# Optimization experiments

Measured on AMD Instinct MI355X. Metric: run time of the kernel, lower is better.

## Reference

```python
import jax, jax.numpy as jnp
import numpy as np

B, S, HID = 1, 2048, 2048
H, NOPE, ROPE, VDIM = 16, 128, 64, 128
QR, KVR = 1536, 512
IH, ID = 16, 128
TOPK = 512
THETA = 10000.0
EPS = 1e-6
SCALE = (NOPE + ROPE) ** -0.5
NEG = -1e9


def _cos_sin(s, dim, dtype):
    inv = 1.0 / (THETA ** (np.arange(0, dim, 2, dtype=np.float32) / dim))
    t = np.arange(s, dtype=np.float32)
    f = np.outer(t, inv)
    emb = np.concatenate([f, f], -1)
    return jnp.asarray(np.cos(emb), dtype), jnp.asarray(np.sin(emb), dtype)


def _rope(x, cos, sin):
    # x: [b,s,h,d]; cos/sin: [s,d]; NeoX-style rotate_half
    x1, x2 = jnp.split(x, 2, axis=-1)
    rot = jnp.concatenate([-x2, x1], axis=-1)
    return x * cos[None, :, None, :] + rot * sin[None, :, None, :]


def _rmsnorm(x, w):
    v = jnp.mean(x.astype(jnp.float32) ** 2, -1, keepdims=True)
    return (x.astype(jnp.float32) * jax.lax.rsqrt(v + EPS)).astype(x.dtype) * w


def _layernorm(x, w, b):
    m = jnp.mean(x, -1, keepdims=True)
    v = jnp.var(x, -1, keepdims=True)
    return (x - m) * jax.lax.rsqrt(v + EPS) * w + b


def setup_inputs() -> dict:
    key = jax.random.key(0)
    ks = jax.random.split(key, 12)
    g = lambda k, shp: jax.random.normal(k, shp, jnp.float32) * 0.02
    return {
        'hidden_states': jax.random.normal(ks[0], (B, S, HID), jnp.float32),
        'q_a_w': g(ks[1], (QR, HID)),
        'q_a_ln_w': jnp.ones((QR,), jnp.float32),
        'q_b_w': g(ks[2], (H * (NOPE + ROPE), QR)),
        'kv_a_w': g(ks[3], (KVR + ROPE, HID)),
        'kv_a_ln_w': jnp.ones((KVR,), jnp.float32),
        'kv_b_w': g(ks[4], (H * (NOPE + VDIM), KVR)),
        'o_w': g(ks[5], (HID, H * VDIM)),
        'idx_wq_b_w': g(ks[6], (IH * ID, QR)),
        'idx_wk_w': g(ks[7], (ID, HID)),
        'idx_kn_w': jnp.ones((ID,), jnp.float32),
        'idx_kn_b': jnp.zeros((ID,), jnp.float32),
        'idx_wproj_w': g(ks[8], (IH, HID)),
    }


def reference(hidden_states, q_a_w, q_a_ln_w, q_b_w, kv_a_w, kv_a_ln_w, kv_b_w, o_w,
              idx_wq_b_w, idx_wk_w, idx_kn_w, idx_kn_b, idx_wproj_w):
    b, s, _ = hidden_states.shape
    cos, sin = _cos_sin(s, ROPE, hidden_states.dtype)

    # --- MLA projections ---
    qr = _rmsnorm(hidden_states @ q_a_w.T, q_a_ln_w)                 # [b,s,QR]
    q = (qr @ q_b_w.T).reshape(b, s, H, NOPE + ROPE)
    q_nope, q_pe = q[..., :NOPE], q[..., NOPE:]
    q_pe = _rope(q_pe, cos, sin)
    ckv = hidden_states @ kv_a_w.T                                   # [b,s,KVR+ROPE]
    c_kv, k_pe = ckv[..., :KVR], ckv[..., KVR:]
    k_pe = _rope(k_pe[:, :, None, :], cos, sin)                      # [b,s,1,ROPE]
    kv = (_rmsnorm(c_kv, kv_a_ln_w) @ kv_b_w.T).reshape(b, s, H, NOPE + VDIM)
    k_nope, v = kv[..., :NOPE], kv[..., NOPE:]

    # --- DSA indexer: per-token importance scores ---
    iq = (qr @ idx_wq_b_w.T).reshape(b, s, IH, ID)
    iq = jnp.concatenate([_rope(iq[..., :ROPE], cos, sin), iq[..., ROPE:]], -1)
    ik = _layernorm(hidden_states @ idx_wk_w.T, idx_kn_w, idx_kn_b)  # [b,s,ID]
    ik_pe = _rope(ik[:, :, None, :ROPE], cos, sin)[:, :, 0, :]
    ik = jnp.concatenate([ik_pe, ik[..., ROPE:]], -1)
    iw = (hidden_states @ idx_wproj_w.T) * (IH ** -0.5)              # [b,s,IH]
    idx_scores = jnp.einsum('bqh,bhqk->bqk', iw,
                            jax.nn.relu(jnp.einsum('bqhd,bkd->bhqk', iq, ik)))
    causal = jnp.tril(jnp.ones((s, s), bool))
    idx_scores = jnp.where(causal[None], idx_scores, -jnp.inf)
    _, top_idx = jax.lax.top_k(idx_scores, TOPK)                     # [b,s,TOPK]
    bi = jnp.arange(b)[:, None, None]
    qi = jnp.arange(s)[None, :, None]
    keep = jnp.zeros((b, s, s), bool).at[bi, qi, top_idx].set(True)
    allowed = keep & causal[None]                                    # [b,s,s]

    # --- sparse top-k attention (top-k mask to -inf before softmax) ---
    qh = jnp.concatenate([q_nope, q_pe], -1)                         # [b,s,H,192]
    kh = jnp.concatenate([k_nope, jnp.broadcast_to(k_pe, (b, s, H, ROPE))], -1)
    scores = jnp.einsum('bqhd,bkhd->bhqk', qh, kh) * SCALE
    scores = jnp.where(allowed[:, None], scores, NEG)
    attn = jax.nn.softmax(scores, -1)
    out = jnp.einsum('bhqk,bkhd->bqhd', attn, v).reshape(b, s, H * VDIM)
    return out @ o_w.T
```

## Files before the change

### kernel.cpp

```cpp
#include <hip/hip_runtime.h>
#include <hip/hip_bf16.h>
#include <math.h>

#define SEQ 2048
#define HIDD 2048
#define QRANK 1536
#define KVRANK 512
#define TOPK 512
#define EPSF 1e-6f
#define SCALE_ATTN 0.07216878364870323f
#define NCAT 1680

typedef __attribute__((ext_vector_type(8))) short short8v;
typedef __attribute__((ext_vector_type(4))) short short4v;
typedef __attribute__((ext_vector_type(4))) float f32x4;

__device__ inline unsigned short f2bf(float f) {
    unsigned u = __float_as_uint(f);
    unsigned r = (u + 0x7FFFu + ((u >> 16) & 1u)) >> 16;
    return (unsigned short)r;
}
__device__ inline float bf2f(unsigned short b) {
    return __uint_as_float(((unsigned)b) << 16);
}
__device__ inline void split2(float x, unsigned short& h, unsigned short& l) {
    h = f2bf(x);
    l = f2bf(x - bf2f(h));
}

__device__ inline short4v ds_read_tr16(const void* p) {
#if __has_builtin(__builtin_amdgcn_ds_read_tr16_b64)
    return __builtin_amdgcn_ds_read_tr16_b64((short4v*)p);
#else
    const unsigned short* u = (const unsigned short*)p;
    short4v r;
    r[0] = (short)u[0]; r[1] = (short)u[16]; r[2] = (short)u[32]; r[3] = (short)u[48];
    return r;
#endif
}

__global__ void rope_table_kernel(float* __restrict__ cos_t, float* __restrict__ sin_t) {
    int s = blockIdx.x;
    int i = threadIdx.x;
    double inv = pow(10000.0, -((double)(2 * i)) / 64.0);
    double f = (double)s * inv;
    cos_t[s * 32 + i] = (float)cos(f);
    sin_t[s * 32 + i] = (float)sin(f);
}

__global__ __launch_bounds__(256) void cvt_bf16_kernel(const float* __restrict__ in,
                                                       unsigned short* __restrict__ out, int n4) {
    for (int i = blockIdx.x * 256 + threadIdx.x; i < n4; i += gridDim.x * 256) {
        float4 v = ((const float4*)in)[i];
        ushort4 o;
        o.x = f2bf(v.x); o.y = f2bf(v.y); o.z = f2bf(v.z); o.w = f2bf(v.w);
        ((ushort4*)out)[i] = o;
    }
}

__global__ __launch_bounds__(256) void wkt_kernel(const float* __restrict__ kvb,
                                                  unsigned short* __restrict__ wkt) {
    int o = blockIdx.x * 256 + threadIdx.x;
    int d = o & 127;
    int n = (o >> 7) & 511;
    int h = o >> 16;
    wkt[o] = f2bf(kvb[((size_t)(h * 256 + d)) * 512 + n]);
}

__global__ __launch_bounds__(256) void khg_kernel(const float* __restrict__ ckvn,
                                                  const float* __restrict__ ckv,
                                                  unsigned short* __restrict__ khg) {
    int s = blockIdx.x;
    for (int i = threadIdx.x; i < 576; i += 256) {
        float v = (i < 512) ? ckvn[(size_t)s * 512 + i] : ckv[(size_t)s * 576 + i];
        khg[(size_t)s * 576 + i] = f2bf(v);
    }
}

__global__ __launch_bounds__(256) void gemm_cat_split_kernel(
    const float* __restrict__ hidden, const float* __restrict__ q_a_w,
    const float* __restrict__ idx_wk_w, const float* __restrict__ idx_wproj_w,
    float* __restrict__ ccat)
{
    __shared__ __align__(16) unsigned short Ah[128 * 32], Al[128 * 32];
    __shared__ __align__(16) unsigned short Bh[128 * 32], Bl[128 * 32];
    int tid = threadIdx.x;
    int l = tid & 63, w = tid >> 6;
    int wr = w >> 1, wc = w & 1;
    int m0 = blockIdx.x * 128, n0 = blockIdx.y * 128;
    f32x4 acc[4][4] = {};
    for (int k0 = 0; k0 < HIDD; k0 += 32) {
        __syncthreads();
#pragma unroll
        for (int i = 0; i < 2; ++i) {
            int idx = tid + i * 256;
            int r = idx >> 2, cc = idx & 3;
            int sw = cc ^ (r & 3);
            {
                const float* src = hidden + (size_t)(m0 + r) * HIDD + k0 + cc * 8;
                float4 f0 = *(const float4*)src, f1 = *(const float4*)(src + 4);
                float xs[8] = {f0.x, f0.y, f0.z, f0.w, f1.x, f1.y, f1.z, f1.w};
                short8v dh, dl;
#pragma unroll
                for (int e = 0; e < 8; ++e) {
                    unsigned short hh, ll; split2(xs[e], hh, ll);
                    dh[e] = (short)hh; dl[e] = (short)ll;
                }
                *(short8v*)&Ah[r * 32 + sw * 8] = dh;
                *(short8v*)&Al[r * 32 + sw * 8] = dl;
            }
            {
                int gb = n0 + r; if (gb > NCAT - 1) gb = NCAT - 1;
                float scale = 1.f;
                const float* src;
                if (gb < 1536) src = q_a_w + (size_t)gb * HIDD;
                else if (gb < 1664) src = idx_wk_w + (size_t)(gb - 1536) * HIDD;
                else { src = idx_wproj_w + (size_t)(gb - 1664) * HIDD; scale = 0.25f; }
                src += k0 + cc * 8;
                float4 f0 = *(const float4*)src, f1 = *(const float4*)(src + 4);
                float xs[8] = {f0.x, f0.y, f0.z, f0.w, f1.x, f1.y, f1.z, f1.w};
                short8v dh, dl;
#pragma unroll
                for (int e = 0; e < 8; ++e) {
                    unsigned short hh, ll; split2(xs[e] * scale, hh, ll);
                    dh[e] = (short)hh; dl[e] = (short)ll;
                }
                *(short8v*)&Bh[r * 32 + sw * 8] = dh;
                *(short8v*)&Bl[r * 32 + sw * 8] = dl;
            }
        }
        __syncthreads();
        short8v avh[4], avl[4];
#pragma unroll
        for (int mt = 0; mt < 4; ++mt) {
            int row = wr * 64 + mt * 16 + (l & 15);
            int ch = (l >> 4) ^ (row & 3);
            avh[mt] = *(const short8v*)&Ah[row * 32 + ch * 8];
            avl[mt] = *(const short8v*)&Al[row * 32 + ch * 8];
        }
#pragma unroll
        for (int nt = 0; nt < 4; ++nt) {
            int row = wc * 64 + nt * 16 + (l & 15);
            int ch = (l >> 4) ^ (row & 3);
            short8v bvh = *(const short8v*)&Bh[row * 32 + ch * 8];
            short8v bvl = *(const short8v*)&Bl[row * 32 + ch * 8];
#pragma unroll
            for (int mt = 0; mt < 4; ++mt) {
                acc[mt][nt] = __builtin_amdgcn_mfma_f32_16x16x32_bf16(avh[mt], bvh, acc[mt][nt], 0, 0, 0);
                acc[mt][nt] = __builtin_amdgcn_mfma_f32_16x16x32_bf16(avh[mt], bvl, acc[mt][nt], 0, 0, 0);
                acc[mt][nt] = __builtin_amdgcn_mfma_f32_16x16x32_bf16(avl[mt], bvh, acc[mt][nt], 0, 0, 0);
            }
        }
    }
#pragma unroll
    for (int mt = 0; mt < 4; ++mt)
#pragma unroll
        for (int nt = 0; nt < 4; ++nt)
#pragma unroll
            for (int i = 0; i < 4; ++i) {
                int gm = m0 + wr * 64 + mt * 16 + (l >> 4) * 4 + i;
                int gn = n0 + wc * 64 + nt * 16 + (l & 15);
                if (gn < NCAT) ccat[(size_t)gm * NCAT + gn] = acc[mt][nt][i];
            }
}

__global__ __launch_bounds__(256) void gemm_iq_split_kernel(
    const float* __restrict__ qr, const float* __restrict__ wq,
    const float* __restrict__ cos_t, const float* __restrict__ sin_t,
    unsigned short* __restrict__ iqh, unsigned short* __restrict__ iql)
{
    __shared__ __align__(16) unsigned short Ah[128 * 32], Al[128 * 32];
    __shared__ __align__(16) unsigned short Bh[128 * 32], Bl[128 * 32];
    int tid = threadIdx.x;
    int l = tid & 63, w = tid >> 6;
    int wr = w >> 1, wc = w & 1;
    int m0 = blockIdx.x * 128, n0 = blockIdx.y * 128;
    int hh_ = blockIdx.y;
    f32x4 acc[4][4] = {};
    for (int k0 = 0; k0 < QRANK; k0 += 32) {
        __syncthreads();
#pragma unroll
        for (int i = 0; i < 2; ++i) {
            int idx = tid + i * 256;
            int r = idx >> 2, cc = idx & 3;
            int sw = cc ^ (r & 3);
            {
                const float* src = qr + (size_t)(m0 + r) * QRANK + k0 + cc * 8;
                float4 f0 = *(const float4*)src, f1 = *(const float4*)(src + 4);
                float xs[8] = {f0.x, f0.y, f0.z, f0.w, f1.x, f1.y, f1.z, f1.w};
                short8v dh, dl;
#pragma unroll
                for (int e = 0; e < 8; ++e) {
                    unsigned short h2, l2; split2(xs[e], h2, l2);
                    dh[e] = (short)h2; dl[e] = (short)l2;
                }
                *(short8v*)&Ah[r * 32 + sw * 8] = dh;
                *(short8v*)&Al[r * 32 + sw * 8] = dl;
            }
            {
                const float* src = wq + (size_t)(n0 + r) * QRANK + k0 + cc * 8;
                float4 f0 = *(const float4*)src, f1 = *(const float4*)(src + 4);
                float xs[8] = {f0.x, f0.y, f0.z, f0.w, f1.x, f1.y, f1.z, f1.w};
                short8v dh, dl;
#pragma unroll
                for (int e = 0; e < 8; ++e) {
                    unsigned short h2, l2; split2(xs[e], h2, l2);
                    dh[e] = (short)h2; dl[e] = (short)l2;
                }
                *(short8v*)&Bh[r * 32 + sw * 8] = dh;
                *(short8v*)&Bl[r * 32 + sw * 8] = dl;
            }
        }
        __syncthreads();
        short8v avh[4], avl[4];
#pragma unroll
        for (int mt = 0; mt < 4; ++mt) {
            int row = wr * 64 + mt * 16 + (l & 15);
            int ch = (l >> 4) ^ (row & 3);
            avh[mt] = *(const short8v*)&Ah[row * 32 + ch * 8];
            avl[mt] = *(const short8v*)&Al[row * 32 + ch * 8];
        }
#pragma unroll
        for (int nt = 0; nt < 4; ++nt) {
            int row = wc * 64 + nt * 16 + (l & 15);
            int ch = (l >> 4) ^ (row & 3);
            short8v bvh = *(const short8v*)&Bh[row * 32 + ch * 8];
            short8v bvl = *(const short8v*)&Bl[row * 32 + ch * 8];
#pragma unroll
            for (int mt = 0; mt < 4; ++mt) {
                acc[mt][nt] = __builtin_amdgcn_mfma_f32_16x16x32_bf16(avh[mt], bvh, acc[mt][nt], 0, 0, 0);
                acc[mt][nt] = __builtin_amdgcn_mfma_f32_16x16x32_bf16(avh[mt], bvl, acc[mt][nt], 0, 0, 0);
                acc[mt][nt] = __builtin_amdgcn_mfma_f32_16x16x32_bf16(avl[mt], bvh, acc[mt][nt], 0, 0, 0);
            }
        }
    }
    if (wc == 0) {
#pragma unroll
        for (int mt = 0; mt < 4; ++mt)
#pragma unroll
            for (int nt = 0; nt < 2; ++nt)
#pragma unroll
                for (int i = 0; i < 4; ++i) {
                    int q = m0 + wr * 64 + mt * 16 + (l >> 4) * 4 + i;
                    int dd = nt * 16 + (l & 15);
                    float c = cos_t[q * 32 + dd], s = sin_t[q * 32 + dd];
                    float x1 = acc[mt][nt][i], x2 = acc[mt][nt + 2][i];
                    acc[mt][nt][i] = x1 * c - x2 * s;
                    acc[mt][nt + 2][i] = x2 * c + x1 * s;
                }
    }
#pragma unroll
    for (int mt = 0; mt < 4; ++mt)
#pragma unroll
        for (int nt = 0; nt < 4; ++nt)
#pragma unroll
            for (int i = 0; i < 4; ++i) {
                int q = m0 + wr * 64 + mt * 16 + (l >> 4) * 4 + i;
                int d = wc * 64 + nt * 16 + (l & 15);
                size_t idx = ((size_t)q * 16 + hh_) * 128 + d;
                unsigned short h2, l2; split2(acc[mt][nt][i], h2, l2);
                iqh[idx] = h2; iql[idx] = l2;
            }
}

template <typename TA, typename TC>
__global__ __launch_bounds__(256) void mfma_nt_kernel(
    const TA* __restrict__ A, const unsigned short* __restrict__ B, TC* __restrict__ C,
    int M, int N, int K, int lda, int ldb, int ldc, long ab, long bb, long cb)
{
    __shared__ __align__(16) unsigned short Asl[128 * 32];
    __shared__ __align__(16) unsigned short Bsl[128 * 32];
    int z = blockIdx.z;
    const TA* Az = A + (size_t)z * ab;
    const unsigned short* Bz = B + (size_t)z * bb;
    TC* Cz = C + (size_t)z * cb;
    int tid = threadIdx.x;
    int l = tid & 63, w = tid >> 6;
    int wr = w >> 1, wc = w & 1;
    int m0 = blockIdx.x * 128, n0 = blockIdx.y * 128;
    f32x4 acc[4][4] = {};

    for (int k0 = 0; k0 < K; k0 += 32) {
        __syncthreads();
#pragma unroll
        for (int i = 0; i < 2; ++i) {
            int idx = tid + i * 256;
            int r = idx >> 2, cc = idx & 3;
            int sw = cc ^ (r & 3);
            {
                short8v d;
                const TA* src = Az + (size_t)(m0 + r) * lda + k0 + cc * 8;
                if constexpr (sizeof(TA) == 2) {
                    d = *(const short8v*)src;
                } else {
                    float4 f0 = *(const float4*)src;
                    float4 f1 = *(const float4*)(src + 4);
                    d[0] = (short)f2bf(f0.x); d[1] = (short)f2bf(f0.y);
                    d[2] = (short)f2bf(f0.z); d[3] = (short)f2bf(f0.w);
                    d[4] = (short)f2bf(f1.x); d[5] = (short)f2bf(f1.y);
                    d[6] = (short)f2bf(f1.z); d[7] = (short)f2bf(f1.w);
                }
                *(short8v*)&Asl[r * 32 + sw * 8] = d;
            }
            {
                int gb = n0 + r; if (gb > N - 1) gb = N - 1;
                short8v d = *(const short8v*)(Bz + (size_t)gb * ldb + k0 + cc * 8);
                *(short8v*)&Bsl[r * 32 + sw * 8] = d;
            }
        }
        __syncthreads();
        short8v av[4], bv[4];
#pragma unroll
        for (int mt = 0; mt < 4; ++mt) {
            int row = wr * 64 + mt * 16 + (l & 15);
            int ch = (l >> 4) ^ (row & 3);
            av[mt] = *(const short8v*)&Asl[row * 32 + ch * 8];
        }
#pragma unroll
        for (int nt = 0; nt < 4; ++nt) {
            int row = wc * 64 + nt * 16 + (l & 15);
            int ch = (l >> 4) ^ (row & 3);
            bv[nt] = *(const short8v*)&Bsl[row * 32 + ch * 8];
        }
#pragma unroll
        for (int mt = 0; mt < 4; ++mt)
#pragma unroll
            for (int nt = 0; nt < 4; ++nt)
                acc[mt][nt] = __builtin_amdgcn_mfma_f32_16x16x32_bf16(av[mt], bv[nt], acc[mt][nt], 0, 0, 0);
    }
#pragma unroll
    for (int mt = 0; mt < 4; ++mt) {
#pragma unroll
        for (int nt = 0; nt < 4; ++nt) {
#pragma unroll
            for (int i = 0; i < 4; ++i) {
                int gm = m0 + wr * 64 + mt * 16 + (l >> 4) * 4 + i;
                int gn = n0 + wc * 64 + nt * 16 + (l & 15);
                if (gn < N) {
                    float v = acc[mt][nt][i];
                    if constexpr (sizeof(TC) == 4) Cz[(size_t)gm * ldc + gn] = v;
                    else Cz[(size_t)gm * ldc + gn] = f2bf(v);
                }
            }
        }
    }
}

__global__ __launch_bounds__(256) void rmsnorm_kernel(
    const float* __restrict__ in, const float* __restrict__ w, float* __restrict__ out,
    unsigned short* __restrict__ bf_out, int n, int in_stride)
{
    int row = blockIdx.x, tid = threadIdx.x;
    const float* x = in + (size_t)row * in_stride;
    float4 v[2];
    int cnt = 0;
    float ss = 0.f;
    int nf4 = n >> 2;
    for (int i = tid; i < nf4; i += 256) {
        float4 t = *(const float4*)(x + i * 4);
        v[cnt++] = t;
        ss += t.x * t.x + t.y * t.y + t.z * t.z + t.w * t.w;
    }
#pragma unroll
    for (int m = 32; m; m >>= 1) ss += __shfl_xor(ss, m);
    __shared__ float red[8];
    int wid = tid >> 6;
    if ((tid & 63) == 0) red[wid] = ss;
    __syncthreads();
    if (tid == 0) {
        float s = red[0] + red[1] + red[2] + red[3];
        red[4] = rsqrtf(s / (float)n + EPSF);
    }
    __syncthreads();
    float scale = red[4];
    cnt = 0;
    for (int i = tid; i < nf4; i += 256) {
        float4 t = v[cnt++];
        float4 wv = *(const float4*)(w + i * 4);
        float4 o;
        o.x = t.x * scale * wv.x; o.y = t.y * scale * wv.y;
        o.z = t.z * scale * wv.z; o.w = t.w * scale * wv.w;
        *(float4*)(out + (size_t)row * n + i * 4) = o;
        if (bf_out) {
            ushort4 ob;
            ob.x = f2bf(o.x); ob.y = f2bf(o.y); ob.z = f2bf(o.z); ob.w = f2bf(o.w);
            *(ushort4*)(bf_out + (size_t)row * n + i * 4) = ob;
        }
    }
}

__global__ __launch_bounds__(64) void ln_rope_split_kernel(
    const float* __restrict__ in, int stride,
    const float* __restrict__ w, const float* __restrict__ b,
    const float* __restrict__ cos_t, const float* __restrict__ sin_t,
    unsigned short* __restrict__ ikh, unsigned short* __restrict__ ikl)
{
    int row = blockIdx.x, tid = threadIdx.x;
    const float* x = in + (size_t)row * stride;
    float x0 = x[tid], x1 = x[tid + 64];
    float s = x0 + x1, ss = x0 * x0 + x1 * x1;
#pragma unroll
    for (int m = 32; m; m >>= 1) { s += __shfl_xor(s, m); ss += __shfl_xor(ss, m); }
    float mean = s * (1.f / 128.f);
    float var = ss * (1.f / 128.f) - mean * mean;
    float r = rsqrtf(var + EPSF);
    float n0 = (x0 - mean) * r * w[tid] + b[tid];
    float n1 = (x1 - mean) * r * w[tid + 64] + b[tid + 64];
    float c = cos_t[row * 32 + (tid & 31)], sn = sin_t[row * 32 + (tid & 31)];
    float other = __shfl_xor(n0, 32);
    float r0 = (tid < 32) ? (n0 * c - other * sn) : (n0 * c + other * sn);
    unsigned short h2, l2;
    split2(r0, h2, l2);
    ikh[(size_t)row * 128 + tid] = h2; ikl[(size_t)row * 128 + tid] = l2;
    split2(n1, h2, l2);
    ikh[(size_t)row * 128 + 64 + tid] = h2; ikl[(size_t)row * 128 + 64 + tid] = l2;
}

__global__ void rope_apply_kernel(
    float* __restrict__ x, const float* __restrict__ cos_t, const float* __restrict__ sin_t,
    int heads, int row_stride, int head_stride, int offset)
{
    int t = blockIdx.x * blockDim.x + threadIdx.x;
    int i = t & 31;
    int hh = (t >> 5) % heads;
    int r = t / (32 * heads);
    if (r >= SEQ) return;
    float* p = x + (size_t)r * row_stride + hh * head_stride + offset;
    float c = cos_t[r * 32 + i], s = sin_t[r * 32 + i];
    float x1 = p[i], x2 = p[i + 32];
    p[i] = x1 * c - x2 * s;
    p[i + 32] = x2 * c + x1 * s;
}

__global__ __launch_bounds__(256) void idx_scores_mfma_kernel(
    const unsigned short* __restrict__ iqh, const unsigned short* __restrict__ iql,
    const unsigned short* __restrict__ ikh, const unsigned short* __restrict__ ikl,
    const float* __restrict__ iwsrc, int iw_stride,
    float* __restrict__ scores)
{
    int q0 = blockIdx.x * 64, k0 = blockIdx.y * 64;
    int tid = threadIdx.x;
    if (k0 > q0 + 63) {
        for (int t = tid; t < 64 * 64; t += 256) {
            int r = t >> 6, c = t & 63;
            scores[(size_t)(q0 + r) * SEQ + k0 + c] = -INFINITY;
        }
        return;
    }
    __shared__ __align__(16) unsigned short skh[64 * 128], skl[64 * 128];
    __shared__ __align__(16) unsigned short sqh[64 * 128], sql[64 * 128];
    __shared__ float iws[64][16];
    int l = tid & 63, w = tid >> 6;
    for (int it = tid; it < 64 * 16; it += 256) {
        int r = it >> 4, c = it & 15;
        int sw = c ^ (r & 15);
        *(short8v*)&skh[r * 128 + sw * 8] = *(const short8v*)(ikh + (size_t)(k0 + r) * 128 + c * 8);
        *(short8v*)&skl[r * 128 + sw * 8] = *(const short8v*)(ikl + (size_t)(k0 + r) * 128 + c * 8);
    }
    {
        int r = tid >> 2, c = tid & 3;
        *(float4*)&iws[r][c * 4] = *(const float4*)(iwsrc + (size_t)(q0 + r) * iw_stride + c * 4);
    }
    f32x4 acc[4] = {};
    for (int h = 0; h < 16; ++h) {
        __syncthreads();
        for (int it = tid; it < 64 * 16; it += 256) {
            int r = it >> 4, c = it & 15;
            int sw = c ^ (r & 15);
            size_t base = ((size_t)(q0 + r) * 16 + h) * 128 + c * 8;
            *(short8v*)&sqh[r * 128 + sw * 8] = *(const short8v*)(iqh + base);
            *(short8v*)&sql[r * 128 + sw * 8] = *(const short8v*)(iql + base);
        }
        __syncthreads();
        f32x4 dot[4] = {};
#pragma unroll
        for (int ks = 0; ks < 4; ++ks) {
            int arow = w * 16 + (l & 15);
            int ach = ((l >> 4) + ks * 4) ^ (arow & 15);
            short8v ah = *(const short8v*)&sqh[arow * 128 + ach * 8];
            short8v al = *(const short8v*)&sql[arow * 128 + ach * 8];
#pragma unroll
            for (int nt = 0; nt < 4; ++nt) {
                int brow = nt * 16 + (l & 15);
                int bch = ((l >> 4) + ks * 4) ^ (brow & 15);
                short8v bh = *(const short8v*)&skh[brow * 128 + bch * 8];
                short8v bl = *(const short8v*)&skl[brow * 128 + bch * 8];
                dot[nt] = __builtin_amdgcn_mfma_f32_16x16x32_bf16(ah, bh, dot[nt], 0, 0, 0);
                dot[nt] = __builtin_amdgcn_mfma_f32_16x16x32_bf16(ah, bl, dot[nt], 0, 0, 0);
                dot[nt] = __builtin_amdgcn_mfma_f32_16x16x32_bf16(al, bh, dot[nt], 0, 0, 0);
            }
        }
#pragma unroll
        for (int nt = 0; nt < 4; ++nt)
#pragma unroll
            for (int i = 0; i < 4; ++i) {
                float wv = iws[w * 16 + (l >> 4) * 4 + i][h];
                acc[nt][i] += wv * fmaxf(dot[nt][i], 0.f);
            }
    }
#pragma unroll
    for (int nt = 0; nt < 4; ++nt)
#pragma unroll
        for (int i = 0; i < 4; ++i) {
            int q = q0 + w * 16 + (l >> 4) * 4 + i;
            int k = k0 + nt * 16 + (l & 15);
            scores[(size_t)q * SEQ + k] = (k <= q) ? acc[nt][i] : -INFINITY;
        }
}

__global__ __launch_bounds__(1024) void topk_kernel(
    const float* __restrict__ scores, int* __restrict__ sel)
{
    int qi = blockIdx.x, tid = threadIdx.x;
    __shared__ unsigned long long keys[2048];
    const float* srow = scores + (size_t)qi * SEQ;
#pragma unroll
    for (int r = 0; r < 2; ++r) {
        int k = tid + r * 1024;
        unsigned u = __float_as_uint(srow[k]);
        unsigned mv = (u & 0x80000000u) ? ~u : (u | 0x80000000u);
        keys[k] = ((unsigned long long)mv << 32) | (unsigned)(2047 - k);
    }
    for (int ksz = 2; ksz <= 2048; ksz <<= 1) {
        for (int j = ksz >> 1; j > 0; j >>= 1) {
            __syncthreads();
#pragma unroll 1
            for (int r = 0; r < 2; ++r) {
                int i = tid + r * 1024;
                int ixj = i ^ j;
                if (ixj > i) {
                    unsigned long long a = keys[i], b = keys[ixj];
                    bool dir = ((i & ksz) == 0);
                    if ((a < b) == dir) { keys[i] = b; keys[ixj] = a; }
                }
            }
        }
    }
    __syncthreads();
    if (tid < TOPK) {
        int k = 2047 - (int)(keys[tid] & 0xFFFFFFFFu);
        sel[(size_t)qi * TOPK + tid] = (tid <= qi) ? k : -1;
    }
}

__global__ __launch_bounds__(256) void attn_mfma_kernel(
    const unsigned short* __restrict__ qabs,
    const float* __restrict__ qsrc,
    const unsigned short* __restrict__ khg,
    const int* __restrict__ sel,
    unsigned short* __restrict__ ocomp)
{
    __shared__ __align__(16) char smem[77568];
    unsigned short* plds = (unsigned short*)(smem + 74752);
    float* smax = (float*)(smem + 76800);
    float* ssum = (float*)(smem + 77056);
    int* selb   = (int*)(smem + 77312);

    const int qi = blockIdx.x;
    const int tid = threadIdx.x;
    const int l = tid & 63, w = tid >> 6;
    const int lg = l >> 4, lr = l & 15;
    const int nv = min(TOPK, qi + 1);
    const int ntile = (nv + 63) >> 6;
    const int krow = w * 16 + lr;

    short8v aq[18];
    {
        const unsigned short* qa = qabs + ((size_t)qi * 16 + lr) * 512 + lg * 8;
#pragma unroll
        for (int ks = 0; ks < 16; ++ks)
            aq[ks] = *(const short8v*)(qa + ks * 32);
        const float* qp = qsrc + (size_t)qi * 3072 + lr * 192 + 128 + lg * 8;
#pragma unroll
        for (int ks = 0; ks < 2; ++ks) {
            float4 f0 = *(const float4*)(qp + ks * 32);
            float4 f1 = *(const float4*)(qp + ks * 32 + 4);
            short8v d;
            d[0] = (short)f2bf(f0.x); d[1] = (short)f2bf(f0.y);
            d[2] = (short)f2bf(f0.z); d[3] = (short)f2bf(f0.w);
            d[4] = (short)f2bf(f1.x); d[5] = (short)f2bf(f1.y);
            d[6] = (short)f2bf(f1.z); d[7] = (short)f2bf(f1.w);
            aq[16 + ks] = d;
        }
    }

    const int sbase = krow * 32 + (lg >> 1) * 2080 + (lg & 1) * 16;
    const int vboff = w * 16640 + lg * 256 + lr * 2;

    float m[4] = {-1e30f, -1e30f, -1e30f, -1e30f};
    float lsum[4] = {0.f, 0.f, 0.f, 0.f};
    f32x4 oacc[8] = {};

    for (int t = 0; t < ntile; ++t) {
        const int j0 = t * 64;
        __syncthreads();
        if (tid < 64) {
            int sv = sel[(size_t)qi * TOPK + j0 + tid];
            selb[tid] = sv < 0 ? 0 : sv;
        }
        __syncthreads();
        for (int it = tid; it < 64 * 64; it += 256) {
            int key = it >> 6, c = it & 63;
            short8v v = *(const short8v*)(khg + (size_t)selb[key] * 576 + c * 8);
            *(short8v*)(smem + (c >> 1) * 2080 + key * 32 + (c & 1) * 16) = v;
        }
        for (int it = tid; it < 64 * 8; it += 256) {
            int key = it >> 3, c = it & 7;
            short8v v = *(const short8v*)(khg + (size_t)selb[key] * 576 + 512 + c * 8);
            *(short8v*)(smem + 66560 + ((key * 128 + c * 16) ^ ((key & 7) << 4))) = v;
        }
        __syncthreads();
        f32x4 s = {};
#pragma unroll
        for (int ks = 0; ks < 16; ++ks) {
            short8v b = *(const short8v*)(smem + sbase + ks * 4160);
            s = __builtin_amdgcn_mfma_f32_16x16x32_bf16(aq[ks], b, s, 0, 0, 0);
        }
#pragma unroll
        for (int ks = 0; ks < 2; ++ks) {
            short8v b = *(const short8v*)(smem + 66560 +
                ((krow * 128 + ks * 64 + lg * 16) ^ ((krow & 7) << 4)));
            s = __builtin_amdgcn_mfma_f32_16x16x32_bf16(aq[16 + ks], b, s, 0, 0, 0);
        }
        bool kvalid = (j0 + krow) < nv;
#pragma unroll
        for (int i = 0; i < 4; ++i)
            s[i] = kvalid ? s[i] * SCALE_ATTN : -1e30f;
        float tm[4];
#pragma unroll
        for (int i = 0; i < 4; ++i) tm[i] = s[i];
#pragma unroll
        for (int sh = 1; sh < 16; sh <<= 1)
#pragma unroll
            for (int i = 0; i < 4; ++i) tm[i] = fmaxf(tm[i], __shfl_xor(tm[i], sh));
        if (lr == 0) *(float4*)&smax[w * 16 + lg * 4] = make_float4(tm[0], tm[1], tm[2], tm[3]);
        __syncthreads();
        float mn[4], scl[4];
#pragma unroll
        for (int i = 0; i < 4; ++i) {
            int h = lg * 4 + i;
            float tmax = fmaxf(fmaxf(smax[h], smax[16 + h]), fmaxf(smax[32 + h], smax[48 + h]));
            mn[i] = fmaxf(m[i], tmax);
            scl[i] = __expf(m[i] - mn[i]);
            m[i] = mn[i];
        }
        float p[4], rs[4];
#pragma unroll
        for (int i = 0; i < 4; ++i) { p[i] = __expf(s[i] - mn[i]); rs[i] = p[i]; }
#pragma unroll
        for (int sh = 1; sh < 16; sh <<= 1)
#pragma unroll
            for (int i = 0; i < 4; ++i) rs[i] += __shfl_xor(rs[i], sh);
        if (lr == 0) *(float4*)&ssum[w * 16 + lg * 4] = make_float4(rs[0], rs[1], rs[2], rs[3]);
        {
            ushort4 pb;
            pb.x = f2bf(p[0]); pb.y = f2bf(p[1]); pb.z = f2bf(p[2]); pb.w = f2bf(p[3]);
            *(ushort4*)&plds[(w * 16 + lr) * 16 + lg * 4] = pb;
        }
        __syncthreads();
#pragma unroll
        for (int i = 0; i < 4; ++i) {
            int h = lg * 4 + i;
            float ts = ssum[h] + ssum[16 + h] + ssum[32 + h] + ssum[48 + h];
            lsum[i] = lsum[i] * scl[i] + ts;
        }
#pragma unroll
        for (int nt = 0; nt < 8; ++nt)
#pragma unroll
            for (int i = 0; i < 4; ++i) oacc[nt][i] *= scl[i];
#pragma unroll
        for (int kb = 0; kb < 2; ++kb) {
            short8v af;
#pragma unroll
            for (int j = 0; j < 8; ++j)
                af[j] = (short)plds[(kb * 32 + lg * 8 + j) * 16 + lr];
#pragma unroll
            for (int nt = 0; nt < 8; ++nt) {
                const char* a = smem + vboff + kb * 1024 + nt * 2080;
                short4v t0 = ds_read_tr16(a);
                short4v t1 = ds_read_tr16(a + 128);
                short8v bf = __builtin_shufflevector(t0, t1, 0, 1, 2, 3, 4, 5, 6, 7);
                oacc[nt] = __builtin_amdgcn_mfma_f32_16x16x32_bf16(af, bf, oacc[nt], 0, 0, 0);
            }
        }
    }
    float inv[4];
#pragma unroll
    for (int i = 0; i < 4; ++i) inv[i] = 1.f / lsum[i];
    unsigned short* ob = ocomp + (size_t)qi * 16 * 512;
#pragma unroll
    for (int nt = 0; nt < 8; ++nt) {
        int d = w * 128 + nt * 16 + lr;
#pragma unroll
        for (int i = 0; i < 4; ++i) {
            int h = lg * 4 + i;
            ob[h * 512 + d] = f2bf(oacc[nt][i] * inv[i]);
        }
    }
}

extern "C" void kernel_launch(void* const* d_in, const int* in_sizes, int n_in,
                              void* d_out, int out_size, void* d_ws, size_t ws_size,
                              hipStream_t stream) {
    (void)in_sizes; (void)n_in; (void)out_size; (void)ws_size;
    const float* hidden      = (const float*)d_in[0];
    const float* q_a_w       = (const float*)d_in[1];
    const float* q_a_ln_w    = (const float*)d_in[2];
    const float* q_b_w       = (const float*)d_in[3];
    const float* kv_a_w      = (const float*)d_in[4];
    const float* kv_a_ln_w   = (const float*)d_in[5];
    const float* kv_b_w      = (const float*)d_in[6];
    const float* o_w         = (const float*)d_in[7];
    const float* idx_wq_b_w  = (const float*)d_in[8];
    const float* idx_wk_w    = (const float*)d_in[9];
    const float* idx_kn_w    = (const float*)d_in[10];
    const float* idx_kn_b    = (const float*)d_in[11];
    const float* idx_wproj_w = (const float*)d_in[12];
    float* out = (float*)d_out;

    char* ws = (char*)d_ws;
    size_t off = 0;
    auto alloc = [&](size_t nbytes) -> void* {
        void* p = ws + off;
        off = (off + nbytes + 255) & ~(size_t)255;
        return p;
    };
    float* cos_t = (float*)alloc((size_t)SEQ * 32 * 4);
    float* sin_t = (float*)alloc((size_t)SEQ * 32 * 4);
    float* qbuf  = (float*)alloc((size_t)SEQ * 3072 * 4);
    float* ckv   = (float*)alloc((size_t)SEQ * 576 * 4);
    float* ckvn  = (float*)alloc((size_t)SEQ * KVRANK * 4);
    int*   sel   = (int*)alloc((size_t)SEQ * TOPK * 4);
    unsigned short* khg      = (unsigned short*)alloc((size_t)SEQ * 576 * 2);
    unsigned short* attno_bf = (unsigned short*)alloc((size_t)SEQ * 2048 * 2);
    unsigned short* qr_bf    = (unsigned short*)alloc((size_t)SEQ * QRANK * 2);
    unsigned short* q_b_bf   = (unsigned short*)alloc((size_t)3072 * QRANK * 2);
    unsigned short* kv_a_bf  = (unsigned short*)alloc((size_t)576 * HIDD * 2);
    unsigned short* o_w_bf   = (unsigned short*)alloc((size_t)HIDD * 2048 * 2);
    unsigned short* kv_b_bf  = (unsigned short*)alloc((size_t)4096 * 512 * 2);
    unsigned short* wkt      = (unsigned short*)alloc((size_t)16 * 512 * 128 * 2);
    size_t mark = off;
    float* qr    = (float*)alloc((size_t)SEQ * QRANK * 4);
    float* ccat  = (float*)alloc((size_t)SEQ * NCAT * 4);
    float* scores = (float*)alloc((size_t)SEQ * SEQ * 4);
    unsigned short* iqh = (unsigned short*)alloc((size_t)SEQ * 2048 * 2);
    unsigned short* iql = (unsigned short*)alloc((size_t)SEQ * 2048 * 2);
    unsigned short* ikh = (unsigned short*)alloc((size_t)SEQ * 128 * 2);
    unsigned short* ikl = (unsigned short*)alloc((size_t)SEQ * 128 * 2);
    off = mark;
    unsigned short* qabsb = (unsigned short*)alloc((size_t)SEQ * 16 * 512 * 2);
    unsigned short* ocomp = (unsigned short*)alloc((size_t)SEQ * 16 * 512 * 2);

    rope_table_kernel<<<dim3(SEQ), dim3(32), 0, stream>>>(cos_t, sin_t);

    cvt_bf16_kernel<<<1024, 256, 0, stream>>>(q_b_w, q_b_bf, 3072 * QRANK / 4);
    cvt_bf16_kernel<<<1024, 256, 0, stream>>>(kv_a_w, kv_a_bf, 576 * HIDD / 4);
    cvt_bf16_kernel<<<1024, 256, 0, stream>>>(o_w, o_w_bf, HIDD * 2048 / 4);
    cvt_bf16_kernel<<<1024, 256, 0, stream>>>(kv_b_w, kv_b_bf, 4096 * 512 / 4);
    wkt_kernel<<<4096, 256, 0, stream>>>(kv_b_w, wkt);

    gemm_cat_split_kernel<<<dim3(16, 14), 256, 0, stream>>>(hidden, q_a_w, idx_wk_w, idx_wproj_w, ccat);

    rmsnorm_kernel<<<SEQ, 256, 0, stream>>>(ccat, q_a_ln_w, qr, qr_bf, QRANK, NCAT);

    ln_rope_split_kernel<<<SEQ, 64, 0, stream>>>(ccat + 1536, NCAT, idx_kn_w, idx_kn_b, cos_t, sin_t, ikh, ikl);

    mfma_nt_kernel<unsigned short, float><<<dim3(16, 24, 1), 256, 0, stream>>>(
        qr_bf, q_b_bf, qbuf, SEQ, 3072, QRANK, QRANK, QRANK, 3072, 0L, 0L, 0L);
    rope_apply_kernel<<<(SEQ * 16 * 32) / 256, 256, 0, stream>>>(qbuf, cos_t, sin_t, 16, 3072, 192, 128);

    mfma_nt_kernel<float, float><<<dim3(16, 5, 1), 256, 0, stream>>>(
        hidden, kv_a_bf, ckv, SEQ, 576, HIDD, HIDD, HIDD, 576, 0L, 0L, 0L);
    rope_apply_kernel<<<(SEQ * 32) / 256, 256, 0, stream>>>(ckv, cos_t, sin_t, 1, 576, 0, 512);
    rmsnorm_kernel<<<SEQ, 256, 0, stream>>>(ckv, kv_a_ln_w, ckvn, nullptr, KVRANK, 576);
    khg_kernel<<<SEQ, 256, 0, stream>>>(ckvn, ckv, khg);

    gemm_iq_split_kernel<<<dim3(16, 16), 256, 0, stream>>>(qr, idx_wq_b_w, cos_t, sin_t, iqh, iql);

    idx_scores_mfma_kernel<<<dim3(32, 32), 256, 0, stream>>>(iqh, iql, ikh, ikl, ccat + 1664, NCAT, scores);
    topk_kernel<<<SEQ, 1024, 0, stream>>>(scores, sel);

    mfma_nt_kernel<float, unsigned short><<<dim3(16, 4, 16), 256, 0, stream>>>(
        qbuf, wkt, qabsb, SEQ, 512, 128, 3072, 128, 16 * 512,
        192L, 512L * 128L, 512L);

    attn_mfma_kernel<<<SEQ, 256, 0, stream>>>(qabsb, qbuf, khg, sel, ocomp);

    mfma_nt_kernel<unsigned short, unsigned short><<<dim3(16, 1, 16), 256, 0, stream>>>(
        ocomp, kv_b_bf + (size_t)128 * 512, attno_bf, SEQ, 128, 512,
        16 * 512, 512, 2048, 512L, 256L * 512L, 128L);

    mfma_nt_kernel<unsigned short, float><<<dim3(16, 16, 1), 256, 0, stream>>>(
        attno_bf, o_w_bf, out, SEQ, HIDD, 2048, 2048, 2048, HIDD, 0L, 0L, 0L);
}
```

Before: 926.7 us.

## Fuse RoPE into GEMM epilogues, merge rmsnorm+bf16 pack, retile attention to 32-key tiles

Applies rotary embedding inside the mfma GEMM epilogue for the q_b and kv_a projections, which removes the separate rope_apply passes over qbuf and ckv. RMSNorm and the bf16 packing of the latent KV are merged into one kernel, dropping the ckvn intermediate. The wkt transpose now goes through a shared-memory tile to get coalesced accesses. The sparse attention kernel moves from 64-key to 32-key tiles with half the LDS, with two waves computing scores under raised priority. This trades more tile iterations and some idle waves for higher occupancy.

```diff
diff --git a/kernel.cpp b/kernel.cpp
--- a/kernel.cpp
+++ b/kernel.cpp
@@ -60,20 +60,22 @@
 
 __global__ __launch_bounds__(256) void wkt_kernel(const float* __restrict__ kvb,
                                                   unsigned short* __restrict__ wkt) {
-    int o = blockIdx.x * 256 + threadIdx.x;
-    int d = o & 127;
-    int n = (o >> 7) & 511;
-    int h = o >> 16;
-    wkt[o] = f2bf(kvb[((size_t)(h * 256 + d)) * 512 + n]);
-}
-
-__global__ __launch_bounds__(256) void khg_kernel(const float* __restrict__ ckvn,
-                                                  const float* __restrict__ ckv,
-                                                  unsigned short* __restrict__ khg) {
-    int s = blockIdx.x;
-    for (int i = threadIdx.x; i < 576; i += 256) {
-        float v = (i < 512) ? ckvn[(size_t)s * 512 + i] : ckv[(size_t)s * 576 + i];
-        khg[(size_t)s * 576 + i] = f2bf(v);
+    __shared__ float t[128][129];
+    int h = blockIdx.x, n0 = blockIdx.y * 128;
+    int tid = threadIdx.x;
+    for (int it = tid; it < 128 * 32; it += 256) {
+        int d = it >> 5, c4 = it & 31;
+        float4 v = *(const float4*)(kvb + ((size_t)(h * 256 + d)) * 512 + n0 + c4 * 4);
+        t[d][c4 * 4 + 0] = v.x; t[d][c4 * 4 + 1] = v.y;
+        t[d][c4 * 4 + 2] = v.z; t[d][c4 * 4 + 3] = v.w;
+    }
+    __syncthreads();
+    for (int it = tid; it < 128 * 32; it += 256) {
+        int n = it >> 5, dc = it & 31;
+        ushort4 o;
+        o.x = f2bf(t[dc * 4 + 0][n]); o.y = f2bf(t[dc * 4 + 1][n]);
+        o.z = f2bf(t[dc * 4 + 2][n]); o.w = f2bf(t[dc * 4 + 3][n]);
+        *(ushort4*)(wkt + ((size_t)h * 512 + n0 + n) * 128 + dc * 4) = o;
     }
 }
 
@@ -266,7 +268,8 @@
 template <typename TA, typename TC>
 __global__ __launch_bounds__(256) void mfma_nt_kernel(
     const TA* __restrict__ A, const unsigned short* __restrict__ B, TC* __restrict__ C,
-    int M, int N, int K, int lda, int ldb, int ldc, long ab, long bb, long cb)
+    int M, int N, int K, int lda, int ldb, int ldc, long ab, long bb, long cb,
+    const float* __restrict__ cos_t, const float* __restrict__ sin_t, int rope_mode)
 {
     __shared__ __align__(16) unsigned short Asl[128 * 32];
     __shared__ __align__(16) unsigned short Bsl[128 * 32];
@@ -328,6 +331,25 @@
             for (int nt = 0; nt < 4; ++nt)
                 acc[mt][nt] = __builtin_amdgcn_mfma_f32_16x16x32_bf16(av[mt], bv[nt], acc[mt][nt], 0, 0, 0);
     }
+    if (rope_mode) {
+        int gcol64 = (n0 >> 6) + wc;
+        bool dorope = (rope_mode == 1) ? ((gcol64 % 3) == 2) : (gcol64 == 8);
+        if (dorope) {
+#pragma unroll
+            for (int mt = 0; mt < 4; ++mt)
+#pragma unroll
+                for (int nt = 0; nt < 2; ++nt)
+#pragma unroll
+                    for (int i = 0; i < 4; ++i) {
+                        int q = m0 + wr * 64 + mt * 16 + (l >> 4) * 4 + i;
+                        int dd = nt * 16 + (l & 15);
+                        float c = cos_t[q * 32 + dd], sn = sin_t[q * 32 + dd];
+                        float x1 = acc[mt][nt][i], x2 = acc[mt][nt + 2][i];
+                        acc[mt][nt][i] = x1 * c - x2 * sn;
+                        acc[mt][nt + 2][i] = x2 * c + x1 * sn;
+                    }
+        }
+    }
 #pragma unroll
     for (int mt = 0; mt < 4; ++mt) {
 #pragma unroll
@@ -389,6 +411,37 @@
     }
 }
 
+__global__ __launch_bounds__(256) void rmsnorm_khg_kernel(
+    const float* __restrict__ ckv, const float* __restrict__ w,
+    unsigned short* __restrict__ khg)
+{
+    int row = blockIdx.x, tid = threadIdx.x;
+    const float* x = ckv + (size_t)row * 576;
+    float4 v = make_float4(0.f, 0.f, 0.f, 0.f);
+    float ss = 0.f;
+    if (tid < 128) {
+        v = *(const float4*)(x + tid * 4);
+        ss = v.x * v.x + v.y * v.y + v.z * v.z + v.w * v.w;
+    }
+#pragma unroll
+    for (int mm = 32; mm; mm >>= 1) ss += __shfl_xor(ss, mm);
+    __shared__ float red[8];
+    if ((tid & 63) == 0) red[tid >> 6] = ss;
+    __syncthreads();
+    if (tid == 0) red[4] = rsqrtf((red[0] + red[1] + red[2] + red[3]) * (1.f / 512.f) + EPSF);
+    __syncthreads();
+    float scale = red[4];
+    if (tid < 128) {
+        float4 wv = *(const float4*)(w + tid * 4);
+        ushort4 ob;
+        ob.x = f2bf(v.x * scale * wv.x); ob.y = f2bf(v.y * scale * wv.y);
+        ob.z = f2bf(v.z * scale * wv.z); ob.w = f2bf(v.w * scale * wv.w);
+        *(ushort4*)(khg + (size_t)row * 576 + tid * 4) = ob;
+    } else if (tid < 192) {
+        khg[(size_t)row * 576 + 512 + (tid - 128)] = f2bf(x[512 + tid - 128]);
+    }
+}
+
 __global__ __launch_bounds__(64) void ln_rope_split_kernel(
     const float* __restrict__ in, int stride,
     const float* __restrict__ w, const float* __restrict__ b,
@@ -416,22 +469,6 @@
     ikh[(size_t)row * 128 + 64 + tid] = h2; ikl[(size_t)row * 128 + 64 + tid] = l2;
 }
 
-__global__ void rope_apply_kernel(
-    float* __restrict__ x, const float* __restrict__ cos_t, const float* __restrict__ sin_t,
-    int heads, int row_stride, int head_stride, int offset)
-{
-    int t = blockIdx.x * blockDim.x + threadIdx.x;
-    int i = t & 31;
-    int hh = (t >> 5) % heads;
-    int r = t / (32 * heads);
-    if (r >= SEQ) return;
-    float* p = x + (size_t)r * row_stride + hh * head_stride + offset;
-    float c = cos_t[r * 32 + i], s = sin_t[r * 32 + i];
-    float x1 = p[i], x2 = p[i + 32];
-    p[i] = x1 * c - x2 * s;
-    p[i + 32] = x2 * c + x1 * s;
-}
-
 __global__ __launch_bounds__(256) void idx_scores_mfma_kernel(
     const unsigned short* __restrict__ iqh, const unsigned short* __restrict__ iql,
     const unsigned short* __restrict__ ikh, const unsigned short* __restrict__ ikl,
@@ -550,18 +587,18 @@
     const int* __restrict__ sel,
     unsigned short* __restrict__ ocomp)
 {
-    __shared__ __align__(16) char smem[77568];
-    unsigned short* plds = (unsigned short*)(smem + 74752);
-    float* smax = (float*)(smem + 76800);
-    float* ssum = (float*)(smem + 77056);
-    int* selb   = (int*)(smem + 77312);
+    __shared__ __align__(16) char smem[39424];
+    unsigned short* plds = (unsigned short*)(smem + 38016);
+    float* smax = (float*)(smem + 39040);
+    float* ssum = (float*)(smem + 39168);
+    int* selb   = (int*)(smem + 39296);
 
     const int qi = blockIdx.x;
     const int tid = threadIdx.x;
     const int l = tid & 63, w = tid >> 6;
     const int lg = l >> 4, lr = l & 15;
     const int nv = min(TOPK, qi + 1);
-    const int ntile = (nv + 63) >> 6;
+    const int ntile = (nv + 31) >> 5;
     const int krow = w * 16 + lr;
 
     short8v aq[18];
@@ -584,105 +621,101 @@
         }
     }
 
-    const int sbase = krow * 32 + (lg >> 1) * 2080 + (lg & 1) * 16;
-    const int vboff = w * 16640 + lg * 256 + lr * 2;
+    const int sbase = krow * 32 + (lg >> 1) * 1056 + (lg & 1) * 16;
+    const int vboff = w * 8 * 1056 + lg * 256 + lr * 2;
 
     float m[4] = {-1e30f, -1e30f, -1e30f, -1e30f};
     float lsum[4] = {0.f, 0.f, 0.f, 0.f};
     f32x4 oacc[8] = {};
 
     for (int t = 0; t < ntile; ++t) {
-        const int j0 = t * 64;
-        __syncthreads();
-        if (tid < 64) {
+        const int j0 = t * 32;
+        __syncthreads();
+        if (tid < 32) {
             int sv = sel[(size_t)qi * TOPK + j0 + tid];
             selb[tid] = sv < 0 ? 0 : sv;
         }
         __syncthreads();
-        for (int it = tid; it < 64 * 64; it += 256) {
+        for (int it = tid; it < 32 * 64; it += 256) {
             int key = it >> 6, c = it & 63;
             short8v v = *(const short8v*)(khg + (size_t)selb[key] * 576 + c * 8);
-            *(short8v*)(smem + (c >> 1) * 2080 + key * 32 + (c & 1) * 16) = v;
-        }
-        for (int it = tid; it < 64 * 8; it += 256) {
-            int key = it >> 3, c = it & 7;
+            *(short8v*)(smem + (c >> 1) * 1056 + key * 32 + (c & 1) * 16) = v;
+        }
+        {
+            int key = tid >> 3, c = tid & 7;
             short8v v = *(const short8v*)(khg + (size_t)selb[key] * 576 + 512 + c * 8);
-            *(short8v*)(smem + 66560 + ((key * 128 + c * 16) ^ ((key & 7) << 4))) = v;
+            *(short8v*)(smem + (32 + (c >> 1)) * 1056 + key * 32 + (c & 1) * 16) = v;
         }
         __syncthreads();
         f32x4 s = {};
-#pragma unroll
-        for (int ks = 0; ks < 16; ++ks) {
-            short8v b = *(const short8v*)(smem + sbase + ks * 4160);
-            s = __builtin_amdgcn_mfma_f32_16x16x32_bf16(aq[ks], b, s, 0, 0, 0);
-        }
-#pragma unroll
-        for (int ks = 0; ks < 2; ++ks) {
-            short8v b = *(const short8v*)(smem + 66560 +
-                ((krow * 128 + ks * 64 + lg * 16) ^ ((krow & 7) << 4)));
-            s = __builtin_amdgcn_mfma_f32_16x16x32_bf16(aq[16 + ks], b, s, 0, 0, 0);
-        }
-        bool kvalid = (j0 + krow) < nv;
-#pragma unroll
-        for (int i = 0; i < 4; ++i)
-            s[i] = kvalid ? s[i] * SCALE_ATTN : -1e30f;
-        float tm[4];
-#pragma unroll
-        for (int i = 0; i < 4; ++i) tm[i] = s[i];
-#pragma unroll
-        for (int sh = 1; sh < 16; sh <<= 1)
-#pragma unroll
-            for (int i = 0; i < 4; ++i) tm[i] = fmaxf(tm[i], __shfl_xor(tm[i], sh));
-        if (lr == 0) *(float4*)&smax[w * 16 + lg * 4] = make_float4(tm[0], tm[1], tm[2], tm[3]);
+        if (w < 2) {
+            __builtin_amdgcn_s_setprio(1);
+#pragma unroll
+            for (int ks = 0; ks < 18; ++ks) {
+                short8v b = *(const short8v*)(smem + sbase + ks * 2112);
+                s = __builtin_amdgcn_mfma_f32_16x16x32_bf16(aq[ks], b, s, 0, 0, 0);
+            }
+            __builtin_amdgcn_s_setprio(0);
+            bool kvalid = (j0 + krow) < nv;
+#pragma unroll
+            for (int i = 0; i < 4; ++i)
+                s[i] = kvalid ? s[i] * SCALE_ATTN : -1e30f;
+            float tm[4];
+#pragma unroll
+            for (int i = 0; i < 4; ++i) tm[i] = s[i];
+#pragma unroll
+            for (int sh = 1; sh < 16; sh <<= 1)
+#pragma unroll
+                for (int i = 0; i < 4; ++i) tm[i] = fmaxf(tm[i], __shfl_xor(tm[i], sh));
+            if (lr == 0) *(float4*)&smax[w * 16 + lg * 4] = make_float4(tm[0], tm[1], tm[2], tm[3]);
+        }
         __syncthreads();
         float mn[4], scl[4];
 #pragma unroll
         for (int i = 0; i < 4; ++i) {
             int h = lg * 4 + i;
-            float tmax = fmaxf(fmaxf(smax[h], smax[16 + h]), fmaxf(smax[32 + h], smax[48 + h]));
+            float tmax = fmaxf(smax[h], smax[16 + h]);
             mn[i] = fmaxf(m[i], tmax);
             scl[i] = __expf(m[i] - mn[i]);
             m[i] = mn[i];
         }
-        float p[4], rs[4];
-#pragma unroll
-        for (int i = 0; i < 4; ++i) { p[i] = __expf(s[i] - mn[i]); rs[i] = p[i]; }
-#pragma unroll
-        for (int sh = 1; sh < 16; sh <<= 1)
-#pragma unroll
-            for (int i = 0; i < 4; ++i) rs[i] += __shfl_xor(rs[i], sh);
-        if (lr == 0) *(float4*)&ssum[w * 16 + lg * 4] = make_float4(rs[0], rs[1], rs[2], rs[3]);
-        {
+        if (w < 2) {
+            float p[4], rs[4];
+#pragma unroll
+            for (int i = 0; i < 4; ++i) { p[i] = __expf(s[i] - mn[i]); rs[i] = p[i]; }
+#pragma unroll
+            for (int sh = 1; sh < 16; sh <<= 1)
+#pragma unroll
+                for (int i = 0; i < 4; ++i) rs[i] += __shfl_xor(rs[i], sh);
+            if (lr == 0) *(float4*)&ssum[w * 16 + lg * 4] = make_float4(rs[0], rs[1], rs[2], rs[3]);
             ushort4 pb;
             pb.x = f2bf(p[0]); pb.y = f2bf(p[1]); pb.z = f2bf(p[2]); pb.w = f2bf(p[3]);
-            *(ushort4*)&plds[(w * 16 + lr) * 16 + lg * 4] = pb;
+            *(ushort4*)&plds[krow * 16 + lg * 4] = pb;
         }
         __syncthreads();
 #pragma unroll
         for (int i = 0; i < 4; ++i) {
             int h = lg * 4 + i;
-            float ts = ssum[h] + ssum[16 + h] + ssum[32 + h] + ssum[48 + h];
-            lsum[i] = lsum[i] * scl[i] + ts;
+            lsum[i] = lsum[i] * scl[i] + (ssum[h] + ssum[16 + h]);
         }
 #pragma unroll
         for (int nt = 0; nt < 8; ++nt)
 #pragma unroll
             for (int i = 0; i < 4; ++i) oacc[nt][i] *= scl[i];
-#pragma unroll
-        for (int kb = 0; kb < 2; ++kb) {
-            short8v af;
-#pragma unroll
-            for (int j = 0; j < 8; ++j)
-                af[j] = (short)plds[(kb * 32 + lg * 8 + j) * 16 + lr];
-#pragma unroll
-            for (int nt = 0; nt < 8; ++nt) {
-                const char* a = smem + vboff + kb * 1024 + nt * 2080;
-                short4v t0 = ds_read_tr16(a);
-                short4v t1 = ds_read_tr16(a + 128);
-                short8v bf = __builtin_shufflevector(t0, t1, 0, 1, 2, 3, 4, 5, 6, 7);
-                oacc[nt] = __builtin_amdgcn_mfma_f32_16x16x32_bf16(af, bf, oacc[nt], 0, 0, 0);
-            }
-        }
+        short8v af;
+#pragma unroll
+        for (int j = 0; j < 8; ++j)
+            af[j] = (short)plds[(lg * 8 + j) * 16 + lr];
+        __builtin_amdgcn_s_setprio(1);
+#pragma unroll
+        for (int nt = 0; nt < 8; ++nt) {
+            const char* a = smem + vboff + nt * 1056;
+            short4v t0 = ds_read_tr16(a);
+            short4v t1 = ds_read_tr16(a + 128);
+            short8v bf = __builtin_shufflevector(t0, t1, 0, 1, 2, 3, 4, 5, 6, 7);
+            oacc[nt] = __builtin_amdgcn_mfma_f32_16x16x32_bf16(af, bf, oacc[nt], 0, 0, 0);
+        }
+        __builtin_amdgcn_s_setprio(0);
     }
     float inv[4];
 #pragma unroll
@@ -729,7 +762,6 @@
     float* sin_t = (float*)alloc((size_t)SEQ * 32 * 4);
     float* qbuf  = (float*)alloc((size_t)SEQ * 3072 * 4);
     float* ckv   = (float*)alloc((size_t)SEQ * 576 * 4);
-    float* ckvn  = (float*)alloc((size_t)SEQ * KVRANK * 4);
     int*   sel   = (int*)alloc((size_t)SEQ * TOPK * 4);
     unsigned short* khg      = (unsigned short*)alloc((size_t)SEQ * 576 * 2);
     unsigned short* attno_bf = (unsigned short*)alloc((size_t)SEQ * 2048 * 2);
@@ -757,7 +789,7 @@
     cvt_bf16_kernel<<<1024, 256, 0, stream>>>(kv_a_w, kv_a_bf, 576 * HIDD / 4);
     cvt_bf16_kernel<<<1024, 256, 0, stream>>>(o_w, o_w_bf, HIDD * 2048 / 4);
     cvt_bf16_kernel<<<1024, 256, 0, stream>>>(kv_b_w, kv_b_bf, 4096 * 512 / 4);
-    wkt_kernel<<<4096, 256, 0, stream>>>(kv_b_w, wkt);
+    wkt_kernel<<<dim3(16, 4), 256, 0, stream>>>(kv_b_w, wkt);
 
     gemm_cat_split_kernel<<<dim3(16, 14), 256, 0, stream>>>(hidden, q_a_w, idx_wk_w, idx_wproj_w, ccat);
 
@@ -766,14 +798,13 @@
     ln_rope_split_kernel<<<SEQ, 64, 0, stream>>>(ccat + 1536, NCAT, idx_kn_w, idx_kn_b, cos_t, sin_t, ikh, ikl);
 
     mfma_nt_kernel<unsigned short, float><<<dim3(16, 24, 1), 256, 0, stream>>>(
-        qr_bf, q_b_bf, qbuf, SEQ, 3072, QRANK, QRANK, QRANK, 3072, 0L, 0L, 0L);
-    rope_apply_kernel<<<(SEQ * 16 * 32) / 256, 256, 0, stream>>>(qbuf, cos_t, sin_t, 16, 3072, 192, 128);
+        qr_bf, q_b_bf, qbuf, SEQ, 3072, QRANK, QRANK, QRANK, 3072, 0L, 0L, 0L,
+        cos_t, sin_t, 1);
 
     mfma_nt_kernel<float, float><<<dim3(16, 5, 1), 256, 0, stream>>>(
-        hidden, kv_a_bf, ckv, SEQ, 576, HIDD, HIDD, HIDD, 576, 0L, 0L, 0L);
-    rope_apply_kernel<<<(SEQ * 32) / 256, 256, 0, stream>>>(ckv, cos_t, sin_t, 1, 576, 0, 512);
-    rmsnorm_kernel<<<SEQ, 256, 0, stream>>>(ckv, kv_a_ln_w, ckvn, nullptr, KVRANK, 576);
-    khg_kernel<<<SEQ, 256, 0, stream>>>(ckvn, ckv, khg);
+        hidden, kv_a_bf, ckv, SEQ, 576, HIDD, HIDD, HIDD, 576, 0L, 0L, 0L,
+        cos_t, sin_t, 2);
+    rmsnorm_khg_kernel<<<SEQ, 256, 0, stream>>>(ckv, kv_a_ln_w, khg);
 
     gemm_iq_split_kernel<<<dim3(16, 16), 256, 0, stream>>>(qr, idx_wq_b_w, cos_t, sin_t, iqh, iql);
 
@@ -782,14 +813,15 @@
 
     mfma_nt_kernel<float, unsigned short><<<dim3(16, 4, 16), 256, 0, stream>>>(
         qbuf, wkt, qabsb, SEQ, 512, 128, 3072, 128, 16 * 512,
-        192L, 512L * 128L, 512L);
+        192L, 512L * 128L, 512L, nullptr, nullptr, 0);
 
     attn_mfma_kernel<<<SEQ, 256, 0, stream>>>(qabsb, qbuf, khg, sel, ocomp);
 
     mfma_nt_kernel<unsigned short, unsigned short><<<dim3(16, 1, 16), 256, 0, stream>>>(
         ocomp, kv_b_bf + (size_t)128 * 512, attno_bf, SEQ, 128, 512,
-        16 * 512, 512, 2048, 512L, 256L * 512L, 128L);
+        16 * 512, 512, 2048, 512L, 256L * 512L, 128L, nullptr, nullptr, 0);
 
     mfma_nt_kernel<unsigned short, float><<<dim3(16, 16, 1), 256, 0, stream>>>(
-        attno_bf, o_w_bf, out, SEQ, HIDD, 2048, 2048, 2048, HIDD, 0L, 0L, 0L);
-}
+        attno_bf, o_w_bf, out, SEQ, HIDD, 2048, 2048, 2048, HIDD, 0L, 0L, 0L,
+        nullptr, nullptr, 0);
+}
```

Result: slower. 960.0 us (+3.6%).
